# Kernel tuning notes

Measured on AMD Instinct MI355X. Metric: run time of the kernel, lower is better.

Reference implementation:

```python
import jax, jax.numpy as jnp
import numpy as np

B, PRE, POST = 32, 2048, 2048
TAU_PRE = 2.0
TAU_POST = 2.0
V_TH = 1.0  # IF-neuron firing threshold


def setup_inputs() -> dict:
    key = jax.random.key(0)
    k1, k2, k3, k4 = jax.random.split(key, 4)
    # input spikes are binary (Bernoulli p=0.2)
    x = (jax.random.uniform(k1, (B, PRE)) < 0.2).astype(jnp.float32)
    # Linear weight [post, pre], Kaiming-ish scale
    W = jax.random.normal(k2, (POST, PRE), dtype=jnp.float32) / np.sqrt(PRE)
    # pre/post traces carried over from previous timesteps
    trace_pre = jax.random.uniform(k3, (B, PRE), dtype=jnp.float32)
    trace_post = jax.random.uniform(k4, (B, POST), dtype=jnp.float32)
    return {"x": x, "W": W, "trace_pre": trace_pre, "trace_post": trace_post}


def reference(x, W, trace_pre, trace_post):
    # connection: i = x @ W^T  -> [B, POST]
    i = x @ W.T
    # node: IF neuron, Heaviside spike
    spike = (i >= V_TH).astype(x.dtype)
    # trace decay (EMA) + spike accumulation
    tp = trace_pre - trace_pre / TAU_PRE + x        # [B, PRE]
    tq = trace_post - trace_post / TAU_POST + spike  # [B, POST]
    # clamp weight once; batch outer-product sums expressed as GEMMs
    Wc = jnp.clip(W, -1.0, 1.0)
    dw = (-Wc * jnp.einsum('bp,bq->pq', tq, x)
          + Wc * jnp.einsum('bp,bq->pq', spike, tp))  # [POST, PRE]
    return (spike, dw)
```

## Files before the change

### kernel.cpp

```cpp
#include <hip/hip_runtime.h>

#define B_ 32
#define PRE_ 2048
#define POST_ 2048
#define QT 8
#define WPAD 2056

typedef __attribute__((ext_vector_type(8))) short short8;
typedef __attribute__((ext_vector_type(4))) short short4v;
typedef __attribute__((ext_vector_type(4))) float floatx4;

__device__ __forceinline__ unsigned short f2bf(float f) {
    unsigned u = __float_as_uint(f);
    u += 0x7FFF + ((u >> 16) & 1);
    return (unsigned short)(u >> 16);
}
__device__ __forceinline__ float bf2f(unsigned short h) {
    return __uint_as_float(((unsigned)h) << 16);
}


__global__ __launch_bounds__(256) void stdp_prep(
    const float* __restrict__ x, const float* __restrict__ trace_pre,
    unsigned short* __restrict__ ws)
{
    int lin  = blockIdx.x * 256 + threadIdx.x;
    int base = lin * 4;
    int b = base >> 11, p = base & 2047;
    floatx4 xv = *(const floatx4*)(x + base);
    floatx4 tv = *(const floatx4*)(trace_pre + base);
    short4v xr;
#pragma unroll
    for (int j = 0; j < 4; ++j) {
        float tp = 0.5f * tv[j] + xv[j];
        unsigned short h = f2bf(tp);
        unsigned short l = f2bf(tp - bf2f(h));
        int o = (p + j) * B_ + b;
        ws[65536 + o]     = h;
        ws[2 * 65536 + o] = l;
        ws[3 * 65536 + o] = f2bf(xv[j]);
        xr[j] = (short)f2bf(xv[j]);
    }
    *(short4v*)(ws + base) = xr;
}

__global__ __launch_bounds__(512) void stdp_fused(
    const float* __restrict__ W, const float* __restrict__ trace_post,
    const unsigned short* __restrict__ ws, float* __restrict__ out)
{
    __shared__ __align__(16) unsigned short Wh[QT * WPAD];
    __shared__ __align__(16) unsigned short Wl[QT * WPAD];
    __shared__ __align__(16) float red[8 * 2 * 4 * 64];
    __shared__ __align__(16) unsigned short spA[QT * 32];
    __shared__ __align__(16) unsigned short nqh[QT * 32];
    __shared__ __align__(16) unsigned short nql[QT * 32];

    const int tid  = threadIdx.x;
    const int wave = tid >> 6, lane = tid & 63;
    const int quad = lane >> 4, l16 = lane & 15;
    const int q0   = blockIdx.x * QT;
    const int qb   = l16 & 7;

#pragma unroll
    for (int it = 0; it < 8; ++it) {
        int id = tid + it * 512;
        int r  = id >> 9;
        int c  = (id & 511) << 2;
        floatx4 wv = *(const floatx4*)(W + (q0 + r) * PRE_ + c);
#pragma unroll
        for (int j = 0; j < 4; ++j) {
            unsigned short h = f2bf(wv[j]);
            Wh[r * WPAD + c + j] = h;
            Wl[r * WPAD + c + j] = f2bf(wv[j] - bf2f(h));
        }
    }
    __syncthreads();

    const unsigned short* xrow = ws;
    floatx4 acc0 = {0.f, 0.f, 0.f, 0.f};
    floatx4 acc1 = {0.f, 0.f, 0.f, 0.f};
#pragma unroll
    for (int s = 0; s < 8; ++s) {
        int ko = wave * 256 + s * 32 + quad * 8;
        short8 a0 = *(const short8*)(xrow + l16 * PRE_ + ko);
        short8 a1 = *(const short8*)(xrow + (16 + l16) * PRE_ + ko);
        short8 bh = *(const short8*)(Wh + qb * WPAD + ko);
        short8 bl = *(const short8*)(Wl + qb * WPAD + ko);
        acc0 = __builtin_amdgcn_mfma_f32_16x16x32_bf16(a0, bh, acc0, 0, 0, 0);
        acc0 = __builtin_amdgcn_mfma_f32_16x16x32_bf16(a0, bl, acc0, 0, 0, 0);
        acc1 = __builtin_amdgcn_mfma_f32_16x16x32_bf16(a1, bh, acc1, 0, 0, 0);
        acc1 = __builtin_amdgcn_mfma_f32_16x16x32_bf16(a1, bl, acc1, 0, 0, 0);
    }
#pragma unroll
    for (int r = 0; r < 4; ++r) {
        red[((wave * 2 + 0) * 4 + r) * 64 + lane] = acc0[r];
        red[((wave * 2 + 1) * 4 + r) * 64 + lane] = acc1[r];
    }
    __syncthreads();

    if (wave < 2 && l16 < QT) {
        int mt = wave;
        int q  = q0 + l16;
#pragma unroll
        for (int r = 0; r < 4; ++r) {
            float s = 0.f;
#pragma unroll
            for (int w = 0; w < 8; ++w) s += red[((w * 2 + mt) * 4 + r) * 64 + lane];
            int b = mt * 16 + quad * 4 + r;
            float spike = (s >= 1.0f) ? 1.0f : 0.0f;
            out[b * POST_ + q] = spike;
            float ntq = -(0.5f * trace_post[b * POST_ + q] + spike);
            unsigned short h = f2bf(ntq);
            unsigned short l = f2bf(ntq - bf2f(h));
            spA[l16 * 32 + b] = f2bf(spike);
            nqh[l16 * 32 + b] = h;
            nql[l16 * 32 + b] = l;
        }
    }
    __syncthreads();

    const unsigned short* tpTh = ws + 65536;
    const unsigned short* tpTl = ws + 2 * 65536;
    const unsigned short* xT   = ws + 3 * 65536;
    float* dw = out + B_ * POST_;

    short8 fs  = *(const short8*)(spA + qb * 32 + quad * 8);
    short8 fnh = *(const short8*)(nqh + qb * 32 + quad * 8);
    short8 fnl = *(const short8*)(nql + qb * 32 + quad * 8);

#pragma unroll 2
    for (int it = 0; it < 16; ++it) {
        int p0 = (wave * 16 + it) * 16;
        int p  = p0 + l16;
        short8 fth = *(const short8*)(tpTh + p * 32 + quad * 8);
        short8 ftl = *(const short8*)(tpTl + p * 32 + quad * 8);
        short8 fx  = *(const short8*)(xT   + p * 32 + quad * 8);
        floatx4 acc = {0.f, 0.f, 0.f, 0.f};
        acc = __builtin_amdgcn_mfma_f32_16x16x32_bf16(fs,  fth, acc, 0, 0, 0);
        acc = __builtin_amdgcn_mfma_f32_16x16x32_bf16(fs,  ftl, acc, 0, 0, 0);
        acc = __builtin_amdgcn_mfma_f32_16x16x32_bf16(fnh, fx,  acc, 0, 0, 0);
        acc = __builtin_amdgcn_mfma_f32_16x16x32_bf16(fnl, fx,  acc, 0, 0, 0);
        if (quad < 2) {
#pragma unroll
            for (int r = 0; r < 4; ++r) {
                int qd = quad * 4 + r;
                float wv = bf2f(Wh[qd * WPAD + p]) + bf2f(Wl[qd * WPAD + p]);
                wv = fminf(fmaxf(wv, -1.0f), 1.0f);
                dw[(q0 + qd) * PRE_ + p] = wv * acc[r];
            }
        }
    }
}

extern "C" void kernel_launch(void* const* d_in, const int* in_sizes, int n_in,
                              void* d_out, int out_size, void* d_ws, size_t ws_size,
                              hipStream_t stream) {
    const float* x     = (const float*)d_in[0];
    const float* W     = (const float*)d_in[1];
    const float* tpre  = (const float*)d_in[2];
    const float* tpost = (const float*)d_in[3];
    float* out = (float*)d_out;
    unsigned short* ws = (unsigned short*)d_ws;

    hipLaunchKernelGGL(stdp_prep, dim3(64), dim3(256), 0, stream, x, tpre, ws);
    hipLaunchKernelGGL(stdp_fused, dim3(POST_ / QT / 1), dim3(512), 0, stream,
                       W, tpost, ws, out);
}
```

Before: 93.76 us.

## Drop bf16 lo-split for traces, interleave fragments, prefetch, remove W-stage barrier

Removes the hi/lo bf16 split for the pre-trace and negated post-trace operands, halving the outer-product MFMAs in the dw phase. Prep now writes tp and x in an interleaved per-p layout with vector stores instead of scattered scalar stores. The fused kernel has each wave stage only the W slice it will read, so the barrier after staging goes away; trace_post is loaded early and the dw loop software-prefetches the next fragments. Rounding tp and tq to a single bf16 lowers the accuracy of dw, which risks failing the tolerance check.

After: 92.53 us. Within noise of the previous version (-1.3%).

```diff
diff --git a/kernel.cpp b/kernel.cpp
--- a/kernel.cpp
+++ b/kernel.cpp
@@ -21,27 +21,30 @@
 
 
 __global__ __launch_bounds__(256) void stdp_prep(
-    const float* __restrict__ x, const float* __restrict__ trace_pre,
+    const float* __restrict__ x, const float* __restrict__ tpre,
     unsigned short* __restrict__ ws)
 {
-    int lin  = blockIdx.x * 256 + threadIdx.x;
+    int lin = blockIdx.x * 256 + threadIdx.x;
     int base = lin * 4;
-    int b = base >> 11, p = base & 2047;
     floatx4 xv = *(const floatx4*)(x + base);
-    floatx4 tv = *(const floatx4*)(trace_pre + base);
     short4v xr;
 #pragma unroll
+    for (int j = 0; j < 4; ++j)
+        xr[j] = (short)(__float_as_uint(xv[j]) >> 16);
+    *(short4v*)(ws + base) = xr;
+
+    int p  = lin >> 3;
+    int b0 = (lin & 7) * 4;
+    short4v tpv, xcv;
+#pragma unroll
     for (int j = 0; j < 4; ++j) {
-        float tp = 0.5f * tv[j] + xv[j];
-        unsigned short h = f2bf(tp);
-        unsigned short l = f2bf(tp - bf2f(h));
-        int o = (p + j) * B_ + b;
-        ws[65536 + o]     = h;
-        ws[2 * 65536 + o] = l;
-        ws[3 * 65536 + o] = f2bf(xv[j]);
-        xr[j] = (short)f2bf(xv[j]);
+        float xx = x[(b0 + j) * PRE_ + p];
+        float tt = tpre[(b0 + j) * PRE_ + p];
+        tpv[j] = (short)f2bf(0.5f * tt + xx);
+        xcv[j] = (short)(__float_as_uint(xx) >> 16);
     }
-    *(short4v*)(ws + base) = xr;
+    *(short4v*)(ws + 65536 + p * 64 + b0) = tpv;
+    *(short4v*)(ws + 65536 + p * 64 + 32 + b0) = xcv;
 }
 
 __global__ __launch_bounds__(512) void stdp_fused(
@@ -51,37 +54,45 @@
     __shared__ __align__(16) unsigned short Wh[QT * WPAD];
     __shared__ __align__(16) unsigned short Wl[QT * WPAD];
     __shared__ __align__(16) float red[8 * 2 * 4 * 64];
-    __shared__ __align__(16) unsigned short spA[QT * 32];
-    __shared__ __align__(16) unsigned short nqh[QT * 32];
-    __shared__ __align__(16) unsigned short nql[QT * 32];
+    __shared__ __align__(16) unsigned short spnq[QT * 64];
 
     const int tid  = threadIdx.x;
     const int wave = tid >> 6, lane = tid & 63;
     const int quad = lane >> 4, l16 = lane & 15;
     const int q0   = blockIdx.x * QT;
     const int qb   = l16 & 7;
+    const int kbase = wave * 256;
 
+    float tpr[4];
+    if (wave < 2 && l16 < QT) {
 #pragma unroll
-    for (int it = 0; it < 8; ++it) {
-        int id = tid + it * 512;
-        int r  = id >> 9;
-        int c  = (id & 511) << 2;
-        floatx4 wv = *(const floatx4*)(W + (q0 + r) * PRE_ + c);
+        for (int r = 0; r < 4; ++r)
+            tpr[r] = trace_post[(wave * 16 + quad * 4 + r) * POST_ + q0 + l16];
+    }
+
+    floatx4 wv[8];
+#pragma unroll
+    for (int r = 0; r < 8; ++r)
+        wv[r] = *(const floatx4*)(W + (q0 + r) * PRE_ + kbase + lane * 4);
+#pragma unroll
+    for (int r = 0; r < 8; ++r) {
+        short4v hv, lv;
 #pragma unroll
         for (int j = 0; j < 4; ++j) {
-            unsigned short h = f2bf(wv[j]);
-            Wh[r * WPAD + c + j] = h;
-            Wl[r * WPAD + c + j] = f2bf(wv[j] - bf2f(h));
+            unsigned short h = f2bf(wv[r][j]);
+            hv[j] = (short)h;
+            lv[j] = (short)f2bf(wv[r][j] - bf2f(h));
         }
+        *(short4v*)&Wh[r * WPAD + kbase + lane * 4] = hv;
+        *(short4v*)&Wl[r * WPAD + kbase + lane * 4] = lv;
     }
-    __syncthreads();
 
     const unsigned short* xrow = ws;
     floatx4 acc0 = {0.f, 0.f, 0.f, 0.f};
     floatx4 acc1 = {0.f, 0.f, 0.f, 0.f};
 #pragma unroll
     for (int s = 0; s < 8; ++s) {
-        int ko = wave * 256 + s * 32 + quad * 8;
+        int ko = kbase + s * 32 + quad * 8;
         short8 a0 = *(const short8*)(xrow + l16 * PRE_ + ko);
         short8 a1 = *(const short8*)(xrow + (16 + l16) * PRE_ + ko);
         short8 bh = *(const short8*)(Wh + qb * WPAD + ko);
@@ -91,6 +102,12 @@
         acc1 = __builtin_amdgcn_mfma_f32_16x16x32_bf16(a1, bh, acc1, 0, 0, 0);
         acc1 = __builtin_amdgcn_mfma_f32_16x16x32_bf16(a1, bl, acc1, 0, 0, 0);
     }
+
+    const unsigned short* frag = ws + 65536;
+    const int pbase = wave * 256;
+    short8 ftp = *(const short8*)(frag + (pbase + l16) * 64 + quad * 8);
+    short8 fx  = *(const short8*)(frag + (pbase + l16) * 64 + 32 + quad * 8);
+
 #pragma unroll
     for (int r = 0; r < 4; ++r) {
         red[((wave * 2 + 0) * 4 + r) * 64 + lane] = acc0[r];
@@ -99,56 +116,47 @@
     __syncthreads();
 
     if (wave < 2 && l16 < QT) {
-        int mt = wave;
-        int q  = q0 + l16;
+        int q = q0 + l16;
 #pragma unroll
         for (int r = 0; r < 4; ++r) {
             float s = 0.f;
 #pragma unroll
-            for (int w = 0; w < 8; ++w) s += red[((w * 2 + mt) * 4 + r) * 64 + lane];
-            int b = mt * 16 + quad * 4 + r;
+            for (int w = 0; w < 8; ++w) s += red[((w * 2 + wave) * 4 + r) * 64 + lane];
+            int b = wave * 16 + quad * 4 + r;
             float spike = (s >= 1.0f) ? 1.0f : 0.0f;
             out[b * POST_ + q] = spike;
-            float ntq = -(0.5f * trace_post[b * POST_ + q] + spike);
-            unsigned short h = f2bf(ntq);
-            unsigned short l = f2bf(ntq - bf2f(h));
-            spA[l16 * 32 + b] = f2bf(spike);
-            nqh[l16 * 32 + b] = h;
-            nql[l16 * 32 + b] = l;
+            float ntq = -(0.5f * tpr[r] + spike);
+            spnq[l16 * 64 + b]      = f2bf(spike);
+            spnq[l16 * 64 + 32 + b] = f2bf(ntq);
         }
     }
     __syncthreads();
 
-    const unsigned short* tpTh = ws + 65536;
-    const unsigned short* tpTl = ws + 2 * 65536;
-    const unsigned short* xT   = ws + 3 * 65536;
+    short8 fs  = *(const short8*)(spnq + qb * 64 + quad * 8);
+    short8 fnq = *(const short8*)(spnq + qb * 64 + 32 + quad * 8);
     float* dw = out + B_ * POST_;
 
-    short8 fs  = *(const short8*)(spA + qb * 32 + quad * 8);
-    short8 fnh = *(const short8*)(nqh + qb * 32 + quad * 8);
-    short8 fnl = *(const short8*)(nql + qb * 32 + quad * 8);
+#pragma unroll 4
+    for (int it = 0; it < 16; ++it) {
+        int pn = (pbase + (((it + 1) & 15) * 16) + l16) * 64;
+        short8 ntp = *(const short8*)(frag + pn + quad * 8);
+        short8 nx  = *(const short8*)(frag + pn + 32 + quad * 8);
 
-#pragma unroll 2
-    for (int it = 0; it < 16; ++it) {
-        int p0 = (wave * 16 + it) * 16;
-        int p  = p0 + l16;
-        short8 fth = *(const short8*)(tpTh + p * 32 + quad * 8);
-        short8 ftl = *(const short8*)(tpTl + p * 32 + quad * 8);
-        short8 fx  = *(const short8*)(xT   + p * 32 + quad * 8);
         floatx4 acc = {0.f, 0.f, 0.f, 0.f};
-        acc = __builtin_amdgcn_mfma_f32_16x16x32_bf16(fs,  fth, acc, 0, 0, 0);
-        acc = __builtin_amdgcn_mfma_f32_16x16x32_bf16(fs,  ftl, acc, 0, 0, 0);
-        acc = __builtin_amdgcn_mfma_f32_16x16x32_bf16(fnh, fx,  acc, 0, 0, 0);
-        acc = __builtin_amdgcn_mfma_f32_16x16x32_bf16(fnl, fx,  acc, 0, 0, 0);
+        acc = __builtin_amdgcn_mfma_f32_16x16x32_bf16(fs,  ftp, acc, 0, 0, 0);
+        acc = __builtin_amdgcn_mfma_f32_16x16x32_bf16(fnq, fx,  acc, 0, 0, 0);
+
+        int p = pbase + it * 16 + l16;
         if (quad < 2) {
 #pragma unroll
             for (int r = 0; r < 4; ++r) {
                 int qd = quad * 4 + r;
-                float wv = bf2f(Wh[qd * WPAD + p]) + bf2f(Wl[qd * WPAD + p]);
-                wv = fminf(fmaxf(wv, -1.0f), 1.0f);
-                dw[(q0 + qd) * PRE_ + p] = wv * acc[r];
+                float wvv = bf2f(Wh[qd * WPAD + p]) + bf2f(Wl[qd * WPAD + p]);
+                wvv = fminf(fmaxf(wvv, -1.0f), 1.0f);
+                dw[(q0 + qd) * PRE_ + p] = wvv * acc[r];
             }
         }
+        ftp = ntp; fx = nx;
     }
 }
 
@@ -163,6 +171,6 @@
     unsigned short* ws = (unsigned short*)d_ws;
 
     hipLaunchKernelGGL(stdp_prep, dim3(64), dim3(256), 0, stream, x, tpre, ws);
-    hipLaunchKernelGGL(stdp_fused, dim3(POST_ / QT / 1), dim3(512), 0, stream,
+    hipLaunchKernelGGL(stdp_fused, dim3(POST_ / QT), dim3(512), 0, stream,
                        W, tpost, ws, out);
 }
```
